# Kernel tuning notes

Measured on AMD Instinct MI355X. Metric: run time of the kernel, lower is better.

Reference implementation:

```python
import jax, jax.numpy as jnp
import numpy as np

ALPHA = 0.2  # LeakyReLU negative slope


def setup_inputs() -> dict:
    key = jax.random.key(0)
    k1, k2, k3, k4 = jax.random.split(key, 4)
    B, N, IN_F, OUT_F = 8, 2048, 128, 64
    inputs = jax.random.normal(k1, (B, N, IN_F), dtype=jnp.float32)
    nodes_embedding = jax.random.normal(k2, (B, N, OUT_F), dtype=jnp.float32)
    # xavier-uniform-like init (gain 1.414)
    limW = 1.414 * np.sqrt(6.0 / (IN_F + OUT_F))
    W = jax.random.uniform(k3, (IN_F, OUT_F), dtype=jnp.float32, minval=-limW, maxval=limW)
    lima = 1.414 * np.sqrt(6.0 / (4 * OUT_F + 1))
    a = jax.random.uniform(k4, (4 * OUT_F, 1), dtype=jnp.float32, minval=-lima, maxval=lima)
    return {"inputs": inputs, "nodes_embedding": nodes_embedding, "W": W, "a": a}


def reference(inputs, nodes_embedding, W, a):
    # x_w: [B,N,F]
    x_w = jnp.matmul(inputs, W)
    # h: [B,N,2F]
    h = jnp.concatenate([nodes_embedding, x_w], axis=2)
    twoF = h.shape[-1]
    # Separable form of concat-based attention: a_input[b,i,j] = [h_i, h_j],
    # so a_input @ a = (h_i . a1) + (h_j . a2). Avoids the O(B*N^2*4F) tensor.
    a1 = a[:twoF, 0]  # [2F]
    a2 = a[twoF:, 0]  # [2F]
    s1 = jnp.einsum('bnf,f->bn', h, a1)  # [B,N]
    s2 = jnp.einsum('bnf,f->bn', h, a2)  # [B,N]
    e = jax.nn.leaky_relu(s1[:, :, None] + s2[:, None, :], negative_slope=ALPHA)  # [B,N,N]
    attention = jax.nn.softmax(e, axis=2)  # softmax over j
    # dropout: eval mode (training=False) -> identity
    h_prime = jnp.matmul(attention, x_w)  # [B,N,F]
    return (jax.nn.relu(h_prime), attention)
```

## Files before the change

### kernel.cpp

```cpp
#include <hip/hip_runtime.h>

#define ALPHA 0.2f
#define B_    8
#define N_    2048
#define INF_  128
#define OUTF_ 64
#define LOG2E 1.4426950408889634f

typedef __attribute__((ext_vector_type(8))) short short8;
typedef __attribute__((ext_vector_type(4))) float f32x4;

__device__ __forceinline__ unsigned short f2bf(float f) {
    unsigned int x = __float_as_uint(f);
    return (unsigned short)((x + 0x7fffu + ((x >> 16) & 1u)) >> 16);
}

__global__ __launch_bounds__(256) void prep_kernel(
    const float* __restrict__ inp,
    const float* __restrict__ nodes,
    const float* __restrict__ Wm,
    const float* __restrict__ av,
    unsigned short* __restrict__ xwT,
    float* __restrict__ s1_out,
    float* __restrict__ s2_out)
{
    __shared__ float w_lds[INF_ * OUTF_];
    __shared__ float in_lds[16 * INF_];
    __shared__ __align__(16) unsigned short t_lds[64 * 16];
    const int tid  = threadIdx.x;
    const int wave = tid >> 6, lane = tid & 63;
    const int r0   = blockIdx.x * 16;

    {
        const float4* Wv = (const float4*)Wm;
        float4* wd = (float4*)w_lds;
        #pragma unroll
        for (int q = 0; q < 8; q++) wd[tid + q * 256] = Wv[tid + q * 256];
        const float4* Iv = (const float4*)(inp + (size_t)r0 * INF_);
        float4* id4 = (float4*)in_lds;
        id4[tid]       = Iv[tid];
        id4[tid + 256] = Iv[tid + 256];
    }
    __syncthreads();

    float acc[4] = {0.f, 0.f, 0.f, 0.f};
    const float* inw = &in_lds[(wave * 4) * INF_];
    #pragma unroll 4
    for (int k = 0; k < INF_; k++) {
        float wv = w_lds[k * OUTF_ + lane];
        acc[0] += inw[k]            * wv;
        acc[1] += inw[INF_ + k]     * wv;
        acc[2] += inw[2 * INF_ + k] * wv;
        acc[3] += inw[3 * INF_ + k] * wv;
    }

    const float a1n = av[lane];
    const float a1x = av[64 + lane];
    const float a2n = av[128 + lane];
    const float a2x = av[192 + lane];

    #pragma unroll
    for (int rr = 0; rr < 4; rr++) {
        const int row = r0 + wave * 4 + rr;
        float nf = nodes[(size_t)row * OUTF_ + lane];
        float p1 = nf * a1n + acc[rr] * a1x;
        float p2 = nf * a2n + acc[rr] * a2x;
        #pragma unroll
        for (int off = 32; off; off >>= 1) {
            p1 += __shfl_down(p1, off);
            p2 += __shfl_down(p2, off);
        }
        if (lane == 0) { s1_out[row] = p1; s2_out[row] = p2; }
        t_lds[lane * 16 + wave * 4 + rr] = f2bf(acc[rr]);
    }
    __syncthreads();

    {
        const int n  = tid >> 2, c0 = (tid & 3) * 4;
        const int b  = r0 >> 11, rb = r0 & (N_ - 1);
        *(uint2*)(xwT + ((size_t)b * OUTF_ + n) * N_ + rb + c0) =
            *(const uint2*)&t_lds[n * 16 + c0];
    }
}

__global__ __launch_bounds__(512, 2) void attn_kernel(
    const unsigned short* __restrict__ xwT,
    const float* __restrict__ s1g,
    const float* __restrict__ s2g,
    float* __restrict__ out_h,
    float* __restrict__ out_att)
{
    __shared__ float s2L[N_];
    __shared__ float s2A[N_];
    __shared__ float s1_lds[64];
    __shared__ float c1_lds[64];
    __shared__ float c2_lds[64];
    __shared__ float redmax[8];
    __shared__ f32x4 redacc[4][64][4];

    const int tid  = threadIdx.x;
    const int wave = tid >> 6, lane = tid & 63;
    const int b  = blockIdx.x & 7;
    const int i0 = (blockIdx.x >> 3) << 6;

    {
        float4 v = *(const float4*)(s2g + b * N_ + tid * 4);
        float lm = fmaxf(fmaxf(v.x, v.y), fmaxf(v.z, v.w));
        *(float4*)&s2L[tid * 4] = make_float4(v.x * LOG2E, v.y * LOG2E,
                                              v.z * LOG2E, v.w * LOG2E);
        *(float4*)&s2A[tid * 4] = make_float4(v.x * (ALPHA * LOG2E), v.y * (ALPHA * LOG2E),
                                              v.z * (ALPHA * LOG2E), v.w * (ALPHA * LOG2E));
        #pragma unroll
        for (int off = 32; off; off >>= 1) lm = fmaxf(lm, __shfl_xor(lm, off));
        if (lane == 0) redmax[wave] = lm;
    }
    if (tid < 64) s1_lds[tid] = s1g[b * N_ + i0 + tid];
    __syncthreads();

    float s2max = redmax[0];
    #pragma unroll
    for (int w = 1; w < 8; w++) s2max = fmaxf(s2max, redmax[w]);

    {
        const int row = tid >> 3, jo = tid & 7;
        const float s1v = s1_lds[row];
        const float vm  = s1v + s2max;
        const float mL  = (vm > 0.f ? vm : ALPHA * vm) * LOG2E;
        const float d1  = s1v * LOG2E - mL;
        const float d2  = s1v * (ALPHA * LOG2E) - mL;
        float l = 0.f;
        for (int j = jo * 4; j < N_; j += 32) {
            float4 xl = *(const float4*)&s2L[j];
            float4 xa = *(const float4*)&s2A[j];
            l += __builtin_amdgcn_exp2f(fmaxf(d1 + xl.x, d2 + xa.x));
            l += __builtin_amdgcn_exp2f(fmaxf(d1 + xl.y, d2 + xa.y));
            l += __builtin_amdgcn_exp2f(fmaxf(d1 + xl.z, d2 + xa.z));
            l += __builtin_amdgcn_exp2f(fmaxf(d1 + xl.w, d2 + xa.w));
        }
        l += __shfl_xor(l, 1);
        l += __shfl_xor(l, 2);
        l += __shfl_xor(l, 4);
        if (jo == 0) {
            const float lg = __builtin_amdgcn_logf(l);
            c1_lds[row] = d1 - lg;
            c2_lds[row] = d2 - lg;
        }
    }
    __syncthreads();

    const int row16 = lane & 15;
    const int quad  = lane >> 4;
    const int wsub  = wave & 3;
    const int jh    = wave >> 2;
    const int irow  = wsub * 16 + row16;
    const float c1  = c1_lds[irow];
    const float c2  = c2_lds[irow];
    const int jb    = jh * 1024;

    const unsigned short* bptr[4];
    #pragma unroll
    for (int g = 0; g < 4; g++)
        bptr[g] = xwT + ((size_t)b * OUTF_ + g * 16 + row16) * N_ + jb + quad * 8;

    float* attp = out_att + ((size_t)(b * N_ + i0 + irow)) * N_ + jb + quad * 8;
    const float* pL = s2L + jb + quad * 8;
    const float* pA = s2A + jb + quad * 8;

    f32x4 acc0 = {0.f,0.f,0.f,0.f}, acc1 = {0.f,0.f,0.f,0.f};
    f32x4 acc2 = {0.f,0.f,0.f,0.f}, acc3 = {0.f,0.f,0.f,0.f};

    uint4 bnext[4];
    #pragma unroll
    for (int g = 0; g < 4; g++) bnext[g] = *(const uint4*)bptr[g];

    for (int jt = 0; jt < 1024; jt += 32) {
        uint4 bc0 = bnext[0], bc1 = bnext[1], bc2 = bnext[2], bc3 = bnext[3];
        const int jn = (jt + 32) & 1023;
        #pragma unroll
        for (int g = 0; g < 4; g++) bnext[g] = *(const uint4*)(bptr[g] + jn);

        float4 sa = *(const float4*)(pL + jt);
        float4 sb = *(const float4*)(pL + jt + 4);
        float4 ta = *(const float4*)(pA + jt);
        float4 tb = *(const float4*)(pA + jt + 4);
        float av8[8];
        av8[0] = __builtin_amdgcn_exp2f(fmaxf(c1 + sa.x, c2 + ta.x));
        av8[1] = __builtin_amdgcn_exp2f(fmaxf(c1 + sa.y, c2 + ta.y));
        av8[2] = __builtin_amdgcn_exp2f(fmaxf(c1 + sa.z, c2 + ta.z));
        av8[3] = __builtin_amdgcn_exp2f(fmaxf(c1 + sa.w, c2 + ta.w));
        av8[4] = __builtin_amdgcn_exp2f(fmaxf(c1 + sb.x, c2 + tb.x));
        av8[5] = __builtin_amdgcn_exp2f(fmaxf(c1 + sb.y, c2 + tb.y));
        av8[6] = __builtin_amdgcn_exp2f(fmaxf(c1 + sb.z, c2 + tb.z));
        av8[7] = __builtin_amdgcn_exp2f(fmaxf(c1 + sb.w, c2 + tb.w));

        *(float4*)(attp + jt)     = make_float4(av8[0], av8[1], av8[2], av8[3]);
        *(float4*)(attp + jt + 4) = make_float4(av8[4], av8[5], av8[6], av8[7]);

        short8 a8;
        #pragma unroll
        for (int jj = 0; jj < 8; jj++) a8[jj] = (short)f2bf(av8[jj]);

        acc0 = __builtin_amdgcn_mfma_f32_16x16x32_bf16(a8, *(short8*)&bc0, acc0, 0, 0, 0);
        acc1 = __builtin_amdgcn_mfma_f32_16x16x32_bf16(a8, *(short8*)&bc1, acc1, 0, 0, 0);
        acc2 = __builtin_amdgcn_mfma_f32_16x16x32_bf16(a8, *(short8*)&bc2, acc2, 0, 0, 0);
        acc3 = __builtin_amdgcn_mfma_f32_16x16x32_bf16(a8, *(short8*)&bc3, acc3, 0, 0, 0);
    }

    if (wave >= 4) {
        redacc[wsub][lane][0] = acc0;
        redacc[wsub][lane][1] = acc1;
        redacc[wsub][lane][2] = acc2;
        redacc[wsub][lane][3] = acc3;
    }
    __syncthreads();
    if (wave < 4) {
        acc0 += redacc[wsub][lane][0];
        acc1 += redacc[wsub][lane][1];
        acc2 += redacc[wsub][lane][2];
        acc3 += redacc[wsub][lane][3];
        const size_t hb = ((size_t)(b * N_) + i0 + wsub * 16) * OUTF_;
        #pragma unroll
        for (int r = 0; r < 4; r++) {
            const size_t ro = hb + (size_t)(quad * 4 + r) * OUTF_ + row16;
            out_h[ro]      = fmaxf(acc0[r], 0.f);
            out_h[ro + 16] = fmaxf(acc1[r], 0.f);
            out_h[ro + 32] = fmaxf(acc2[r], 0.f);
            out_h[ro + 48] = fmaxf(acc3[r], 0.f);
        }
    }
}

extern "C" void kernel_launch(void* const* d_in, const int* in_sizes, int n_in,
                              void* d_out, int out_size, void* d_ws, size_t ws_size,
                              hipStream_t stream) {
    const float* inp   = (const float*)d_in[0];
    const float* nodes = (const float*)d_in[1];
    const float* Wm    = (const float*)d_in[2];
    const float* av    = (const float*)d_in[3];

    float* out_h   = (float*)d_out;
    float* out_att = out_h + (size_t)B_ * N_ * OUTF_;

    unsigned short* xwT = (unsigned short*)d_ws;
    float* s1_ws = (float*)((char*)d_ws + (size_t)B_ * OUTF_ * N_ * sizeof(unsigned short));
    float* s2_ws = s1_ws + (size_t)B_ * N_;

    prep_kernel<<<(B_ * N_) / 16, 256, 0, stream>>>(inp, nodes, Wm, av,
                                                    xwT, s1_ws, s2_ws);
    attn_kernel<<<256, 512, 0, stream>>>(xwT, s1_ws, s2_ws, out_h, out_att);
}
```

Before: 187.4 us.

## Split attention j-range across 16 waves and use packed bf16 convert

```diff
diff --git a/kernel.cpp b/kernel.cpp
--- a/kernel.cpp
+++ b/kernel.cpp
@@ -13,6 +13,12 @@
 __device__ __forceinline__ unsigned short f2bf(float f) {
     unsigned int x = __float_as_uint(f);
     return (unsigned short)((x + 0x7fffu + ((x >> 16) & 1u)) >> 16);
+}
+
+__device__ __forceinline__ unsigned int cvtpk_bf16(float lo, float hi) {
+    unsigned int r;
+    asm("v_cvt_pk_bf16_f32 %0, %1, %2" : "=v"(r) : "v"(lo), "v"(hi));
+    return r;
 }
 
 __global__ __launch_bounds__(256) void prep_kernel(
@@ -83,20 +89,22 @@
     }
 }
 
-__global__ __launch_bounds__(512, 2) void attn_kernel(
+__global__ __launch_bounds__(1024, 4) void attn_kernel(
     const unsigned short* __restrict__ xwT,
     const float* __restrict__ s1g,
     const float* __restrict__ s2g,
     float* __restrict__ out_h,
     float* __restrict__ out_att)
 {
-    __shared__ float s2L[N_];
-    __shared__ float s2A[N_];
+    __shared__ __align__(16) float smem[12288];
     __shared__ float s1_lds[64];
     __shared__ float c1_lds[64];
     __shared__ float c2_lds[64];
-    __shared__ float redmax[8];
-    __shared__ f32x4 redacc[4][64][4];
+    __shared__ float redmax[16];
+
+    float* s2L = smem;
+    float* s2A = smem + 2048;
+    f32x4* red = (f32x4*)smem;
 
     const int tid  = threadIdx.x;
     const int wave = tid >> 6, lane = tid & 63;
@@ -104,12 +112,12 @@
     const int i0 = (blockIdx.x >> 3) << 6;
 
     {
-        float4 v = *(const float4*)(s2g + b * N_ + tid * 4);
-        float lm = fmaxf(fmaxf(v.x, v.y), fmaxf(v.z, v.w));
-        *(float4*)&s2L[tid * 4] = make_float4(v.x * LOG2E, v.y * LOG2E,
-                                              v.z * LOG2E, v.w * LOG2E);
-        *(float4*)&s2A[tid * 4] = make_float4(v.x * (ALPHA * LOG2E), v.y * (ALPHA * LOG2E),
-                                              v.z * (ALPHA * LOG2E), v.w * (ALPHA * LOG2E));
+        float2 v = *(const float2*)(s2g + b * N_ + tid * 2);
+        float lm = fmaxf(v.x, v.y);
+        s2L[tid * 2]     = v.x * LOG2E;
+        s2L[tid * 2 + 1] = v.y * LOG2E;
+        s2A[tid * 2]     = v.x * (ALPHA * LOG2E);
+        s2A[tid * 2 + 1] = v.y * (ALPHA * LOG2E);
         #pragma unroll
         for (int off = 32; off; off >>= 1) lm = fmaxf(lm, __shfl_xor(lm, off));
         if (lane == 0) redmax[wave] = lm;
@@ -119,17 +127,17 @@
 
     float s2max = redmax[0];
     #pragma unroll
-    for (int w = 1; w < 8; w++) s2max = fmaxf(s2max, redmax[w]);
-
-    {
-        const int row = tid >> 3, jo = tid & 7;
+    for (int w = 1; w < 16; w++) s2max = fmaxf(s2max, redmax[w]);
+
+    {
+        const int row = tid >> 4, jo = tid & 15;
         const float s1v = s1_lds[row];
         const float vm  = s1v + s2max;
         const float mL  = (vm > 0.f ? vm : ALPHA * vm) * LOG2E;
         const float d1  = s1v * LOG2E - mL;
         const float d2  = s1v * (ALPHA * LOG2E) - mL;
         float l = 0.f;
-        for (int j = jo * 4; j < N_; j += 32) {
+        for (int j = jo * 4; j < N_; j += 64) {
             float4 xl = *(const float4*)&s2L[j];
             float4 xa = *(const float4*)&s2A[j];
             l += __builtin_amdgcn_exp2f(fmaxf(d1 + xl.x, d2 + xa.x));
@@ -140,6 +148,7 @@
         l += __shfl_xor(l, 1);
         l += __shfl_xor(l, 2);
         l += __shfl_xor(l, 4);
+        l += __shfl_xor(l, 8);
         if (jo == 0) {
             const float lg = __builtin_amdgcn_logf(l);
             c1_lds[row] = d1 - lg;
@@ -151,11 +160,11 @@
     const int row16 = lane & 15;
     const int quad  = lane >> 4;
     const int wsub  = wave & 3;
-    const int jh    = wave >> 2;
+    const int jq    = wave >> 2;
     const int irow  = wsub * 16 + row16;
     const float c1  = c1_lds[irow];
     const float c2  = c2_lds[irow];
-    const int jb    = jh * 1024;
+    const int jb    = jq * 512;
 
     const unsigned short* bptr[4];
     #pragma unroll
@@ -173,9 +182,9 @@
     #pragma unroll
     for (int g = 0; g < 4; g++) bnext[g] = *(const uint4*)bptr[g];
 
-    for (int jt = 0; jt < 1024; jt += 32) {
+    for (int jt = 0; jt < 512; jt += 32) {
         uint4 bc0 = bnext[0], bc1 = bnext[1], bc2 = bnext[2], bc3 = bnext[3];
-        const int jn = (jt + 32) & 1023;
+        const int jn = (jt + 32) & 511;
         #pragma unroll
         for (int g = 0; g < 4; g++) bnext[g] = *(const uint4*)(bptr[g] + jn);
 
@@ -196,9 +205,12 @@
         *(float4*)(attp + jt)     = make_float4(av8[0], av8[1], av8[2], av8[3]);
         *(float4*)(attp + jt + 4) = make_float4(av8[4], av8[5], av8[6], av8[7]);
 
-        short8 a8;
-        #pragma unroll
-        for (int jj = 0; jj < 8; jj++) a8[jj] = (short)f2bf(av8[jj]);
+        uint4 pk;
+        pk.x = cvtpk_bf16(av8[0], av8[1]);
+        pk.y = cvtpk_bf16(av8[2], av8[3]);
+        pk.z = cvtpk_bf16(av8[4], av8[5]);
+        pk.w = cvtpk_bf16(av8[6], av8[7]);
+        short8 a8 = *(short8*)&pk;
 
         acc0 = __builtin_amdgcn_mfma_f32_16x16x32_bf16(a8, *(short8*)&bc0, acc0, 0, 0, 0);
         acc1 = __builtin_amdgcn_mfma_f32_16x16x32_bf16(a8, *(short8*)&bc1, acc1, 0, 0, 0);
@@ -206,18 +218,18 @@
         acc3 = __builtin_amdgcn_mfma_f32_16x16x32_bf16(a8, *(short8*)&bc3, acc3, 0, 0, 0);
     }
 
-    if (wave >= 4) {
-        redacc[wsub][lane][0] = acc0;
-        redacc[wsub][lane][1] = acc1;
-        redacc[wsub][lane][2] = acc2;
-        redacc[wsub][lane][3] = acc3;
-    }
-    __syncthreads();
-    if (wave < 4) {
-        acc0 += redacc[wsub][lane][0];
-        acc1 += redacc[wsub][lane][1];
-        acc2 += redacc[wsub][lane][2];
-        acc3 += redacc[wsub][lane][3];
+    __syncthreads();
+    if (jq > 0) {
+        f32x4* p = red + (((jq - 1) * 4 + wsub) * 64 + lane) * 4;
+        p[0] = acc0; p[1] = acc1; p[2] = acc2; p[3] = acc3;
+    }
+    __syncthreads();
+    if (jq == 0) {
+        #pragma unroll
+        for (int q = 0; q < 3; q++) {
+            f32x4* p = red + ((q * 4 + wsub) * 64 + lane) * 4;
+            acc0 += p[0]; acc1 += p[1]; acc2 += p[2]; acc3 += p[3];
+        }
         const size_t hb = ((size_t)(b * N_) + i0 + wsub * 16) * OUTF_;
         #pragma unroll
         for (int r = 0; r < 4; r++) {
@@ -247,5 +259,5 @@
 
     prep_kernel<<<(B_ * N_) / 16, 256, 0, stream>>>(inp, nodes, Wm, av,
                                                     xwT, s1_ws, s2_ws);
-    attn_kernel<<<256, 512, 0, stream>>>(xwT, s1_ws, s2_ws, out_h, out_att);
-}
+    attn_kernel<<<256, 1024, 0, stream>>>(xwT, s1_ws, s2_ws, out_h, out_att);
+}
```

Result: no change. 187.7 us (+0.2%).
